# Performance work log

Measured on AMD Instinct MI355X. Metric: run time of the kernel, lower is better.

The kernel has to match this reference:

```python
import jax, jax.numpy as jnp
import numpy as np

B, S, C_IN, E, H, DFF = 16, 1024, 4, 128, 8, 512
C1 = E * 4
DH = E // H
EPS = 1e-5


def _layer_norm(x, g, b):
    m = x.mean(-1, keepdims=True)
    v = ((x - m) ** 2).mean(-1, keepdims=True)
    return (x - m) / jnp.sqrt(v + EPS) * g + b


def _forward(x, conv1_w, conv1_b, bn1_g, bn1_b, bn1_m, bn1_v,
             conv2_w, conv2_b, bn2_g, bn2_b, bn2_m, bn2_v,
             wq, wk, wv, rel_bias, ln_attn_g, ln_attn_b,
             ln1_g, ln1_b, ff_w1, ff_b1, ff_w2, ff_b2, ln2_g, ln2_b):
    b, s, _ = x.shape
    dn = ('NCHW', 'OIHW', 'NCHW')
    h = x.transpose(0, 2, 1)[:, None]                      # [B,1,4,S]
    # Conv2d(1, 512, [1,8], padding='same') -> torch pads (3,4) on width
    h = jax.lax.conv_general_dilated(h, conv1_w, (1, 1), [(0, 0), (3, 4)], dimension_numbers=dn)
    h = h + conv1_b[None, :, None, None]
    h = (h - bn1_m[None, :, None, None]) * (bn1_g / jnp.sqrt(bn1_v + EPS))[None, :, None, None] + bn1_b[None, :, None, None]
    h = jax.nn.gelu(h, approximate=False)                  # [B,512,4,S]
    # Conv2d(512, 128, [4,1], padding='valid') collapses channel axis
    h = jax.lax.conv_general_dilated(h, conv2_w, (1, 1), [(0, 0), (0, 0)], dimension_numbers=dn)
    h = h + conv2_b[None, :, None, None]
    h = (h - bn2_m[None, :, None, None]) * (bn2_g / jnp.sqrt(bn2_v + EPS))[None, :, None, None] + bn2_b[None, :, None, None]
    h = jax.nn.gelu(h, approximate=False)                  # [B,128,1,S]
    x_src = h[:, :, 0, :].transpose(0, 2, 1)               # [B,S,E]
    # tAPE fixed positional encoding (sin/cos scaled by E/S)
    pos = jnp.arange(s, dtype=x.dtype)[:, None]
    div = jnp.exp(jnp.arange(0, E, 2, dtype=x.dtype) * (-np.log(10000.0) / E))
    ang = pos * div * (E / s)
    pe = jnp.zeros((s, E), x.dtype).at[:, 0::2].set(jnp.sin(ang)).at[:, 1::2].set(jnp.cos(ang))
    xp = x_src + pe
    # eRPE attention (Attention_Rel_Scl): scale = emb_size**-0.5, bias added POST-softmax
    q = (xp @ wq.T).reshape(b, s, H, DH).transpose(0, 2, 1, 3)
    k = (xp @ wk.T).reshape(b, s, H, DH).transpose(0, 2, 1, 3)
    v = (xp @ wv.T).reshape(b, s, H, DH).transpose(0, 2, 1, 3)
    attn = jax.nn.softmax(jnp.einsum('bhid,bhjd->bhij', q, k) * (E ** -0.5), axis=-1)
    idx = jnp.arange(s)[:, None] - jnp.arange(s)[None, :] + (s - 1)   # [S,S] in [0, 2S-2]
    attn = attn + rel_bias[idx].transpose(2, 0, 1)[None]   # [1,H,S,S]
    o = jnp.einsum('bhij,bhjd->bhid', attn, v).transpose(0, 2, 1, 3).reshape(b, s, E)
    o = _layer_norm(o, ln_attn_g, ln_attn_b)               # to_out = LayerNorm
    att = _layer_norm(x_src + o, ln1_g, ln1_b)
    ff = jax.nn.relu(att @ ff_w1.T + ff_b1) @ ff_w2.T + ff_b2
    out = _layer_norm(att + ff, ln2_g, ln2_b)
    return out.mean(axis=1)                                # GAP + flatten -> [B,E]


def setup_inputs():
    key = jax.random.key(0)
    ks = jax.random.split(key, 16)
    f32 = jnp.float32
    return {
        'x': jax.random.normal(ks[0], (B, S, C_IN), f32),
        'conv1_w': jax.random.normal(ks[1], (C1, 1, 1, 8), f32) * 0.1,
        'conv1_b': jnp.zeros((C1,), f32),
        'bn1_g': jnp.ones((C1,), f32), 'bn1_b': jnp.zeros((C1,), f32),
        'bn1_m': jax.random.normal(ks[2], (C1,), f32) * 0.01,
        'bn1_v': jax.random.uniform(ks[3], (C1,), f32, 0.5, 1.5),
        'conv2_w': jax.random.normal(ks[4], (E, C1, C_IN, 1), f32) * 0.02,
        'conv2_b': jnp.zeros((E,), f32),
        'bn2_g': jnp.ones((E,), f32), 'bn2_b': jnp.zeros((E,), f32),
        'bn2_m': jax.random.normal(ks[5], (E,), f32) * 0.01,
        'bn2_v': jax.random.uniform(ks[6], (E,), f32, 0.5, 1.5),
        'wq': jax.random.normal(ks[7], (E, E), f32) * (E ** -0.5),
        'wk': jax.random.normal(ks[8], (E, E), f32) * (E ** -0.5),
        'wv': jax.random.normal(ks[9], (E, E), f32) * (E ** -0.5),
        'rel_bias': jax.random.normal(ks[10], (2 * S - 1, H), f32) * 0.02,
        'ln_attn_g': jnp.ones((E,), f32), 'ln_attn_b': jnp.zeros((E,), f32),
        'ln1_g': jnp.ones((E,), f32), 'ln1_b': jnp.zeros((E,), f32),
        'ff_w1': jax.random.normal(ks[11], (DFF, E), f32) * (E ** -0.5),
        'ff_b1': jnp.zeros((DFF,), f32),
        'ff_w2': jax.random.normal(ks[12], (E, DFF), f32) * (DFF ** -0.5),
        'ff_b2': jnp.zeros((E,), f32),
        'ln2_g': jnp.ones((E,), f32), 'ln2_b': jnp.zeros((E,), f32),
    }


def reference(x, conv1_w, conv1_b, bn1_g, bn1_b, bn1_m, bn1_v,
              conv2_w, conv2_b, bn2_g, bn2_b, bn2_m, bn2_v,
              wq, wk, wv, rel_bias, ln_attn_g, ln_attn_b,
              ln1_g, ln1_b, ff_w1, ff_b1, ff_w2, ff_b2, ln2_g, ln2_b):
    return _forward(x, conv1_w, conv1_b, bn1_g, bn1_b, bn1_m, bn1_v,
                    conv2_w, conv2_b, bn2_g, bn2_b, bn2_m, bn2_v,
                    wq, wk, wv, rel_bias, ln_attn_g, ln_attn_b,
                    ln1_g, ln1_b, ff_w1, ff_b1, ff_w2, ff_b2, ln2_g, ln2_b)
```

## Files before the change

kernel.cpp:

```cpp
#include <hip/hip_runtime.h>
#include <hip/hip_bf16.h>
#include <math.h>

using bf16 = __hip_bfloat16;
typedef unsigned short u16;
typedef unsigned int u32;
typedef const float* __restrict__ cfp;
typedef const u16* __restrict__ cbu;

typedef __attribute__((ext_vector_type(8))) short short8v;
typedef __attribute__((ext_vector_type(4))) float f32x4;
typedef __attribute__((ext_vector_type(16))) float f32x16;

static constexpr int kS = 1024, kE = 128, kH = 8, kDH = 16, kDFF = 512;
static constexpr float kEps = 1e-5f;

__device__ __forceinline__ float geluf(float x) { return 0.5f * x * (1.f + erff(x * 0.70710678118654752f)); }
__device__ __forceinline__ float gelu_fast(float x) {
  float x2 = x * x;
  float u2 = 1.5957691216057308f * x * fmaf(0.044715f, x2, 1.f);
  float t = __expf(u2);
  return fmaf(-x, __frcp_rn(t + 1.f), x);
}
__device__ __forceinline__ u16 f2b(float f) {
  u32 u = __float_as_uint(f);
  u32 r = (u + 0x7FFFu + ((u >> 16) & 1u)) >> 16;
  return (u16)r;
}

template<int N> __device__ __forceinline__ void wait_vmcnt() {
  asm volatile("s_waitcnt vmcnt(%0)" :: "n"(N) : "memory");
  __builtin_amdgcn_sched_barrier(0);
}

__global__ __launch_bounds__(256) void setup_kernel(
    cfp x, cfp w1, cfp c1b, cfp g1, cfp b1, cfp m1, cfp v1, u16* __restrict__ Abuf,
    cfp w2, u16* __restrict__ w2b, cfp relb, u16* __restrict__ T,
    cfp fw2, u16* __restrict__ w2fb, float* __restrict__ dout,
    cfp wq, cfp wk, cfp wv, u16* __restrict__ wqkvb,
    cfp fw1, u16* __restrict__ w1fb) {
  int tid = threadIdx.x;
  if (blockIdx.x < 2048) {
    __shared__ float xs[15][4];
    int row0 = blockIdx.x * 8;
    int b = row0 >> 10, s0 = row0 & 1023;
    if (tid < 15) {
      int gs = s0 - 3 + tid;
      float4 xv = (gs >= 0 && gs < kS) ? ((const float4*)x)[b * kS + gs]
                                       : make_float4(0.f, 0.f, 0.f, 0.f);
      xs[tid][0] = xv.x; xs[tid][1] = xv.y; xs[tid][2] = xv.z; xs[tid][3] = xv.w;
    }
    __syncthreads();

    float w[2][8], sc[2], ofs[2], cb[2];
#pragma unroll
    for (int cc = 0; cc < 2; ++cc) {
      int cx = tid * 2 + cc;
#pragma unroll
      for (int t = 0; t < 8; ++t) w[cc][t] = w1[cx * 8 + t];
      sc[cc] = g1[cx] * __frsqrt_rn(v1[cx] + kEps);
      ofs[cc] = b1[cx] - m1[cx] * sc[cc];
      cb[cc] = c1b[cx];
    }

    for (int rl = 0; rl < 8; ++rl) {
      float ev[8];
#pragma unroll
      for (int cc = 0; cc < 2; ++cc) {
#pragma unroll
        for (int rr = 0; rr < 4; ++rr) {
          float h = cb[cc];
#pragma unroll
          for (int t = 0; t < 8; ++t) h += xs[rl + t][rr] * w[cc][t];
          ev[cc * 4 + rr] = gelu_fast(h * sc[cc] + ofs[cc]);
        }
      }
      uint4 pk;
      asm("v_cvt_pk_bf16_f32 %0, %1, %2" : "=v"(pk.x) : "v"(ev[0]), "v"(ev[1]));
      asm("v_cvt_pk_bf16_f32 %0, %1, %2" : "=v"(pk.y) : "v"(ev[2]), "v"(ev[3]));
      asm("v_cvt_pk_bf16_f32 %0, %1, %2" : "=v"(pk.z) : "v"(ev[4]), "v"(ev[5]));
      asm("v_cvt_pk_bf16_f32 %0, %1, %2" : "=v"(pk.w) : "v"(ev[6]), "v"(ev[7]));
      int ck = (tid & ~7) | ((tid & 7) ^ (rl & 7));
      *(uint4*)(Abuf + (size_t)(row0 + rl) * 2048 + ck * 8) = pk;
    }
    return;
  }

  int bid = blockIdx.x - 2048;
  if (bid < 128) {
    int n = bid, ck = tid;
    const float* src = w2 + (size_t)n * 2048 + (size_t)ck * 8;
    float4 a = *(const float4*)src;
    float4 b = *(const float4*)(src + 4);
    short8v sv;
    sv[0] = (short)f2b(a.x); sv[1] = (short)f2b(a.y);
    sv[2] = (short)f2b(a.z); sv[3] = (short)f2b(a.w);
    sv[4] = (short)f2b(b.x); sv[5] = (short)f2b(b.y);
    sv[6] = (short)f2b(b.z); sv[7] = (short)f2b(b.w);
    int cd = (ck & ~7) | ((ck & 7) ^ (n & 7));
    *(short8v*)(w2b + (size_t)n * 2048 + cd * 8) = sv;
  } else if (bid < 380) {
    int idx = (bid - 128) * 4 + (tid >> 6);
    int l = tid & 63;
    int h = idx / 126, t = idx - h * 126;
    int lr = l & 15, lg = l >> 4;
    short8v v;
#pragma unroll
    for (int e = 0; e < 8; ++e) {
      int ix = 16 * t + 31 + lr - 8 * lg - e;
      v[e] = (short)f2b(relb[ix * 8 + h]);
    }
    *(short8v*)(T + ((size_t)(h * 126 + t) * 64 + l) * 8) = v;
  } else if (bid < 412) {
    int n = (bid - 380) * 4 + (tid >> 6);
    int ck = tid & 63;
    const float* src = fw2 + (size_t)n * 512 + (size_t)ck * 8;
    float4 a = *(const float4*)src;
    float4 b = *(const float4*)(src + 4);
    short8v sv;
    sv[0] = (short)f2b(a.x); sv[1] = (short)f2b(a.y);
    sv[2] = (short)f2b(a.z); sv[3] = (short)f2b(a.w);
    sv[4] = (short)f2b(b.x); sv[5] = (short)f2b(b.y);
    sv[6] = (short)f2b(b.z); sv[7] = (short)f2b(b.w);
    int cd = (ck & ~7) | ((ck & 7) ^ (n & 7));
    *(short8v*)(w2fb + (size_t)n * 512 + cd * 8) = sv;
  } else if (bid < 413) {
#pragma unroll
    for (int e = 0; e < 8; ++e) dout[tid * 8 + e] = 0.f;
  } else if (bid < 437) {
    int g = (bid - 413) * 256 + tid;
    int z = g >> 11, local = g & 2047;
    const float* src = ((z == 0) ? wq : (z == 1) ? wk : wv) + (size_t)local * 8;
    float4 a = *(const float4*)src;
    float4 b = *(const float4*)(src + 4);
    short8v sv;
    sv[0] = (short)f2b(a.x); sv[1] = (short)f2b(a.y);
    sv[2] = (short)f2b(a.z); sv[3] = (short)f2b(a.w);
    sv[4] = (short)f2b(b.x); sv[5] = (short)f2b(b.y);
    sv[6] = (short)f2b(b.z); sv[7] = (short)f2b(b.w);
    *(short8v*)(wqkvb + (size_t)z * 16384 + local * 8) = sv;
  } else {
    int g = (bid - 437) * 256 + tid;
    const float* src = fw1 + (size_t)g * 8;
    float4 a = *(const float4*)src;
    float4 b = *(const float4*)(src + 4);
    short8v sv;
    sv[0] = (short)f2b(a.x); sv[1] = (short)f2b(a.y);
    sv[2] = (short)f2b(a.z); sv[3] = (short)f2b(a.w);
    sv[4] = (short)f2b(b.x); sv[5] = (short)f2b(b.y);
    sv[6] = (short)f2b(b.z); sv[7] = (short)f2b(b.w);
    *(short8v*)(w1fb + (size_t)g * 8) = sv;
  }
}

__global__ __launch_bounds__(256, 2) void convgemm_kernel(
    const u16* __restrict__ Abuf, const u16* __restrict__ w2b,
    cfp c2b, cfp g2, cfp b2, cfp m2, cfp v2,
    float* __restrict__ xsrc, u16* __restrict__ xpeb) {
  __shared__ short8v lds[3840];
  const int tid = threadIdx.x;
  const int mtile = blockIdx.x;
  const int wid = tid >> 6, lane = tid & 63;
  const int lrow = lane & 15, lk = lane >> 4;
  const int m0w = (wid & 1) * 16, n0w = (wid >> 1) * 64;

  float scn[4], cc[4], dv[4];
#pragma unroll
  for (int ni = 0; ni < 4; ++ni) {
    int n = n0w + ni * 16 + lrow;
    scn[ni] = g2[n] * __frsqrt_rn(v2[n] + kEps);
    cc[ni] = (c2b[n] - m2[n]) * scn[ni] + b2[n];
    dv[ni] = __expf((float)(n >> 1) * (-0.14391156824963732f)) * 0.125f;
  }

  f32x4 acc[4];
#pragma unroll
  for (int ni = 0; ni < 4; ++ni) acc[ni] = (f32x4){0.f, 0.f, 0.f, 0.f};

  const int q = wid * 64 + lane;
  const u16* aG = Abuf + (size_t)(mtile * 32 + (q >> 3)) * 2048 + (q & 7) * 8;

  auto stage = [&](int t) {
    int buf = t % 3;
    short8v* A = lds + buf * 1280;
    __builtin_amdgcn_global_load_lds(
        (const __attribute__((address_space(1))) void*)(aG + t * 64),
        (__attribute__((address_space(3))) void*)(A + wid * 64), 16, 0, 0);
#pragma unroll
    for (int r = 0; r < 4; ++r) {
      int qq = r * 256 + q;
      const u16* g = w2b + (size_t)(qq >> 3) * 2048 + t * 64 + (qq & 7) * 8;
      __builtin_amdgcn_global_load_lds(
          (const __attribute__((address_space(1))) void*)g,
          (__attribute__((address_space(3))) void*)(A + 256 + r * 256 + wid * 64), 16, 0, 0);
    }
  };

  auto compute = [&](int t) {
    int buf = t % 3;
    const short8v* A = lds + buf * 1280;
    const short8v* B = A + 256;
#pragma unroll
    for (int ks = 0; ks < 2; ++ks) {
      int ar = m0w + lrow;
      u32 ao = ((u32)(ar * 128 + ks * 64 + lk * 16)) ^ ((u32)((ar & 7) << 4));
      short8v af = A[ao >> 4];
#pragma unroll
      for (int ni = 0; ni < 4; ++ni) {
        int br = n0w + ni * 16 + lrow;
        u32 bo = ((u32)(br * 128 + ks * 64 + lk * 16)) ^ ((u32)((br & 7) << 4));
        short8v bf = B[bo >> 4];
        acc[ni] = __builtin_amdgcn_mfma_f32_16x16x32_bf16(af, bf, acc[ni], 0, 0, 0);
      }
    }
  };

  stage(0); stage(1); stage(2);
  for (int t = 0; t < 30; ++t) {
    wait_vmcnt<10>();
    __builtin_amdgcn_s_barrier();
    __builtin_amdgcn_sched_barrier(0);
    compute(t);
    asm volatile("" ::: "memory");
    __builtin_amdgcn_s_barrier();
    __builtin_amdgcn_sched_barrier(0);
    if (t <= 28) stage(t + 3);
  }
  wait_vmcnt<5>();
  __builtin_amdgcn_s_barrier();
  __builtin_amdgcn_sched_barrier(0);
  compute(30);
  asm volatile("" ::: "memory");
  __builtin_amdgcn_s_barrier();
  __builtin_amdgcn_sched_barrier(0);
  wait_vmcnt<0>();
  __builtin_amdgcn_s_barrier();
  __builtin_amdgcn_sched_barrier(0);
  compute(31);

#pragma unroll
  for (int ni = 0; ni < 4; ++ni) {
    int n = n0w + ni * 16 + lrow;
#pragma unroll
    for (int r = 0; r < 4; ++r) {
      int grow = mtile * 32 + m0w + lk * 4 + r;
      float gv = geluf(acc[ni][r] * scn[ni] + cc[ni]);
      xsrc[(size_t)grow * kE + n] = gv;
      int s = grow & 1023;
      float ang = (float)s * dv[ni];
      float pe = (n & 1) ? __cosf(ang) : __sinf(ang);
      xpeb[(size_t)grow * kE + n] = f2b(gv + pe);
    }
  }
}

template<int ASRC, int MODE, int KTOT, int BM>
__global__ __launch_bounds__(256, 4) void gemm_kernel(
    const void* __restrict__ Ap, cbu Wf,
    cfp p0, cbu p1, cbu p2,
    void* __restrict__ Out, cfp res, int mbase) {
  constexpr int MI = BM / 32;
  __shared__ short8v Ab[BM * 8];
  __shared__ short8v Bb[512];

  int tid = threadIdx.x;
  int mtile = blockIdx.x, ntile = blockIdx.y;

  cbu Wsel = Wf;
  if (MODE == 1) Wsel = (blockIdx.z == 0) ? Wf : ((blockIdx.z == 1) ? p1 : p2);

  int wid = tid >> 6, lane = tid & 63;
  int m0w = (wid >> 1) * (BM / 2), n0w = (wid & 1) * 32;
  int lrow = lane & 15, lk = lane >> 4;

  f32x4 acc[MI][2];
#pragma unroll
  for (int mi = 0; mi < MI; ++mi)
#pragma unroll
    for (int ni = 0; ni < 2; ++ni) acc[mi][ni] = (f32x4){0.f, 0.f, 0.f, 0.f};

  for (int k0 = 0; k0 < KTOT; k0 += 64) {
    __syncthreads();
#pragma unroll
    for (int c = 0; c < BM / 32; ++c) {
      int chunk = tid + 256 * c;
      int row = chunk >> 3, kc = chunk & 7;
      int arow = mtile * BM + row;
      u32 off = ((u32)(row * 128 + kc * 16)) ^ ((u32)((row & 7) << 4));
      const u16* As = (const u16*)Ap + (size_t)arow * KTOT + k0 + kc * 8;
      Ab[off >> 4] = *(const short8v*)As;
    }
#pragma unroll
    for (int c = 0; c < 2; ++c) {
      int chunk = tid + 256 * c;
      int row = chunk >> 3, kc = chunk & 7;
      const u16* Wp = Wsel + (size_t)(ntile * 64 + row) * KTOT + k0 + kc * 8;
      u32 off = ((u32)(row * 128 + kc * 16)) ^ ((u32)((row & 7) << 4));
      Bb[off >> 4] = *(const short8v*)Wp;
    }
    __syncthreads();
#pragma unroll
    for (int ks = 0; ks < 2; ++ks) {
      short8v af[MI], bfr[2];
#pragma unroll
      for (int mi = 0; mi < MI; ++mi) {
        int row = m0w + mi * 16 + lrow;
        u32 off = ((u32)(row * 128 + ks * 64 + lk * 16)) ^ ((u32)((row & 7) << 4));
        af[mi] = Ab[off >> 4];
      }
#pragma unroll
      for (int ni = 0; ni < 2; ++ni) {
        int row = n0w + ni * 16 + lrow;
        u32 off = ((u32)(row * 128 + ks * 64 + lk * 16)) ^ ((u32)((row & 7) << 4));
        bfr[ni] = Bb[off >> 4];
      }
#pragma unroll
      for (int mi = 0; mi < MI; ++mi)
#pragma unroll
        for (int ni = 0; ni < 2; ++ni)
          acc[mi][ni] = __builtin_amdgcn_mfma_f32_16x16x32_bf16(af[mi], bfr[ni], acc[mi][ni], 0, 0, 0);
    }
  }

  const float qsc = 0.088388347648318447f * 1.4426950408889634f;
#pragma unroll
  for (int ni = 0; ni < 2; ++ni) {
    int n = ntile * 64 + n0w + ni * 16 + lrow;
    float c0 = 0.f;
    if (MODE == 2) c0 = p0[n];
#pragma unroll
    for (int mi = 0; mi < MI; ++mi) {
#pragma unroll
      for (int r = 0; r < 4; ++r) {
        int grow = mbase + mtile * BM + m0w + mi * 16 + lk * 4 + r;
        float val = acc[mi][ni][r];
        if (MODE == 1) {
          if (blockIdx.z == 0) val *= qsc;
          int s = grow & 1023, b_ = grow >> 10;
          u16* ob = (u16*)Out + (size_t)blockIdx.z * 2097152;
          ob[(((size_t)(b_ * kH + (n >> 4))) * kS + s) * kDH + (n & 15)] = f2b(val);
        } else if (MODE == 2) {
          int np = (n & ~56) | ((((n >> 3) ^ grow) & 7) << 3);
          ((u16*)Out)[(size_t)grow * kDFF + np] = f2b(fmaxf(val + c0, 0.f));
        }
      }
    }
  }
}

__global__ __launch_bounds__(256, 2) void ff2ln_kernel(
    const u16* __restrict__ Abuf, const u16* __restrict__ w2fb,
    cfp fb2, cfp l2g, cfp l2b, cfp res, float* __restrict__ dout) {
  __shared__ short8v lds[3840];
  __shared__ float st1[2][32], st2[2][32];
  __shared__ float red[128];
  const int tid = threadIdx.x;
  const int mtile = blockIdx.x;
  const int wid = tid >> 6, lane = tid & 63;
  const int lrow = lane & 15, lk = lane >> 4;
  const int m0w = (wid & 1) * 16, n0w = (wid >> 1) * 64;
  if (tid < 128) red[tid] = 0.f;

  float c0[4], gg[4], bb[4];
#pragma unroll
  for (int ni = 0; ni < 4; ++ni) {
    int n = n0w + ni * 16 + lrow;
    c0[ni] = fb2[n]; gg[ni] = l2g[n]; bb[ni] = l2b[n];
  }

  f32x4 acc[4];
#pragma unroll
  for (int ni = 0; ni < 4; ++ni) acc[ni] = (f32x4){0.f, 0.f, 0.f, 0.f};

  const int q = wid * 64 + lane;
  const u16* aG = Abuf + (size_t)(mtile * 32 + (q >> 3)) * 512 + (q & 7) * 8;

  auto stage = [&](int t) {
    int buf = t % 3;
    short8v* A = lds + buf * 1280;
    __builtin_amdgcn_global_load_lds(
        (const __attribute__((address_space(1))) void*)(aG + t * 64),
        (__attribute__((address_space(3))) void*)(A + wid * 64), 16, 0, 0);
#pragma unroll
    for (int r = 0; r < 4; ++r) {
      int qq = r * 256 + q;
      const u16* g = w2fb + (size_t)(qq >> 3) * 512 + t * 64 + (qq & 7) * 8;
      __builtin_amdgcn_global_load_lds(
          (const __attribute__((address_space(1))) void*)g,
          (__attribute__((address_space(3))) void*)(A + 256 + r * 256 + wid * 64), 16, 0, 0);
    }
  };

  auto compute = [&](int t) {
    int buf = t % 3;
    const short8v* A = lds + buf * 1280;
    const short8v* B = A + 256;
#pragma unroll
    for (int ks = 0; ks < 2; ++ks) {
      int ar = m0w + lrow;
      u32 ao = ((u32)(ar * 128 + ks * 64 + lk * 16)) ^ ((u32)((ar & 7) << 4));
      short8v af = A[ao >> 4];
#pragma unroll
      for (int ni = 0; ni < 4; ++ni) {
        int br = n0w + ni * 16 + lrow;
        u32 bo = ((u32)(br * 128 + ks * 64 + lk * 16)) ^ ((u32)((br & 7) << 4));
        short8v bf = B[bo >> 4];
        acc[ni] = __builtin_amdgcn_mfma_f32_16x16x32_bf16(af, bf, acc[ni], 0, 0, 0);
      }
    }
  };

  stage(0); stage(1); stage(2);
  for (int t = 0; t < 6; ++t) {
    wait_vmcnt<10>();
    __builtin_amdgcn_s_barrier();
    __builtin_amdgcn_sched_barrier(0);
    compute(t);
    asm volatile("" ::: "memory");
    __builtin_amdgcn_s_barrier();
    __builtin_amdgcn_sched_barrier(0);
    if (t <= 4) stage(t + 3);
  }
  wait_vmcnt<5>();
  __builtin_amdgcn_s_barrier();
  __builtin_amdgcn_sched_barrier(0);
  compute(6);
  asm volatile("" ::: "memory");
  __builtin_amdgcn_s_barrier();
  __builtin_amdgcn_sched_barrier(0);
  wait_vmcnt<0>();
  __builtin_amdgcn_s_barrier();
  __builtin_amdgcn_sched_barrier(0);
  compute(7);

  float y[4][4];
  float s1[4] = {0.f, 0.f, 0.f, 0.f}, s2[4] = {0.f, 0.f, 0.f, 0.f};
#pragma unroll
  for (int ni = 0; ni < 4; ++ni) {
    int n = n0w + ni * 16 + lrow;
#pragma unroll
    for (int r = 0; r < 4; ++r) {
      int grow = mtile * 32 + m0w + lk * 4 + r;
      float v = acc[ni][r] + c0[ni] + res[(size_t)grow * kE + n];
      y[ni][r] = v;
      s1[r] += v;
      s2[r] += v * v;
    }
  }
#pragma unroll
  for (int r = 0; r < 4; ++r) {
    for (int off = 1; off < 16; off <<= 1) {
      s1[r] += __shfl_xor(s1[r], off);
      s2[r] += __shfl_xor(s2[r], off);
    }
  }
  __syncthreads();
  if (lrow == 0) {
#pragma unroll
    for (int r = 0; r < 4; ++r) {
      int ridx = m0w + lk * 4 + r;
      st1[wid >> 1][ridx] = s1[r];
      st2[wid >> 1][ridx] = s2[r];
    }
  }
  __syncthreads();
  float colsum[4] = {0.f, 0.f, 0.f, 0.f};
#pragma unroll
  for (int r = 0; r < 4; ++r) {
    int ridx = m0w + lk * 4 + r;
    float t1 = st1[0][ridx] + st1[1][ridx];
    float t2 = st2[0][ridx] + st2[1][ridx];
    float mean = t1 * (1.f / 128.f);
    float var = t2 * (1.f / 128.f) - mean * mean;
    float inv = __frsqrt_rn(var + kEps);
#pragma unroll
    for (int ni = 0; ni < 4; ++ni)
      colsum[ni] += (y[ni][r] - mean) * inv * gg[ni] + bb[ni];
  }
#pragma unroll
  for (int ni = 0; ni < 4; ++ni) {
    colsum[ni] += __shfl_xor(colsum[ni], 16);
    colsum[ni] += __shfl_xor(colsum[ni], 32);
  }
  if (lk == 0) {
#pragma unroll
    for (int ni = 0; ni < 4; ++ni)
      atomicAdd(&red[n0w + ni * 16 + lrow], colsum[ni]);
  }
  __syncthreads();
  int b = mtile >> 5;
  if (tid < 128) atomicAdd(&dout[b * kE + tid], red[tid] * (1.f / 1024.f));
}

__global__ __launch_bounds__(512, 2) void attn_kernel(
    const u16* __restrict__ qb, const u16* __restrict__ kb,
    const u16* __restrict__ vb, const u16* __restrict__ rbT,
    float* __restrict__ o) {
  __shared__ u16 Vsh[16 * 1032];
  __shared__ u16 Pt[8][1280];

  int tid = threadIdx.x;
  int bid = blockIdx.x;
  int quarter = bid >> 7;
  int bb = (bid >> 3) & 15;
  int h = bid & 7;
  size_t base = (size_t)(bb * kH + h) * (kS * kDH);

  for (int j = tid; j < 1024; j += 512) {
    const uint4* src = (const uint4*)(vb + base + j * 16);
    uint4 a = src[0], b = src[1];
    u32 wv[8] = {a.x, a.y, a.z, a.w, b.x, b.y, b.z, b.w};
#pragma unroll
    for (int p = 0; p < 8; ++p) {
      Vsh[(2 * p) * 1032 + j]     = (u16)(wv[p] & 0xFFFFu);
      Vsh[(2 * p + 1) * 1032 + j] = (u16)(wv[p] >> 16);
    }
  }
  __syncthreads();

  int w = tid >> 6, l = tid & 63;
  int lr = l & 15, lg = l >> 4;
  int q32 = l & 31, hi = l >> 5;
  u16* P = Pt[w];
  int q0w = quarter * 256 + w * 32;
  int tbase = (q0w + 992) >> 4;
  const u16* rbh = rbT + (size_t)h * 126 * 512;

  short8v qf = *(const short8v*)(qb + base + (size_t)(q0w + q32) * 16 + hi * 8);
  short8v ones;
#pragma unroll
  for (int e = 0; e < 8; ++e) ones[e] = (short)0x3F80;

  f32x4 acc_e[2], acc_rb[2], acc_l[2];
#pragma unroll
  for (int qt = 0; qt < 2; ++qt) {
    acc_e[qt] = (f32x4){0.f, 0.f, 0.f, 0.f};
    acc_rb[qt] = (f32x4){0.f, 0.f, 0.f, 0.f};
    acc_l[qt] = (f32x4){0.f, 0.f, 0.f, 0.f};
  }
  const f32x16 z16 = {0.f,0.f,0.f,0.f,0.f,0.f,0.f,0.f,0.f,0.f,0.f,0.f,0.f,0.f,0.f,0.f};

  const u16* kfp = kb + base + (size_t)q32 * 16 + hi * 8;
  const u16* rfp = rbh + (size_t)tbase * 512 + l * 8;

  short8v kf_c = *(const short8v*)kfp;
  short8v rf0_c = *(const short8v*)rfp;
  short8v rf1_c = *(const short8v*)(rfp + 512);

  const int wswz = (q32 >> 3) & 3;
  const int c0r = lg ^ ((lr >> 3) & 3);
  const int c1r = lg ^ (((16 + lr) >> 3) & 3);

  for (int jb = 0; jb < 32; ++jb) {
    short8v kf_n, rf0_n, rf1_n;
    if (jb < 31) {
      kf_n = *(const short8v*)(kfp + (size_t)(jb + 1) * 512);
      const u16* rp = rfp - (size_t)(jb + 1) * 1024;
      rf0_n = *(const short8v*)rp;
      rf1_n = *(const short8v*)(rp + 512);
    }
    f32x16 s = __builtin_amdgcn_mfma_f32_32x32x16_bf16(kf_c, qf, z16, 0, 0, 0);
    float ev[16];
#pragma unroll
    for (int r = 0; r < 16; ++r) ev[r] = __builtin_amdgcn_exp2f(s[r]);
#pragma unroll
    for (int rq = 0; rq < 4; ++rq) {
      u32 p0, p1;
      asm("v_cvt_pk_bf16_f32 %0, %1, %2" : "=v"(p0) : "v"(ev[4 * rq]), "v"(ev[4 * rq + 1]));
      asm("v_cvt_pk_bf16_f32 %0, %1, %2" : "=v"(p1) : "v"(ev[4 * rq + 2]), "v"(ev[4 * rq + 3]));
      *(uint2*)(P + q32 * 40 + (rq ^ wswz) * 8 + hi * 4) = make_uint2(p0, p1);
    }
    short8v vf = *(const short8v*)(Vsh + lr * 1032 + jb * 32 + lg * 8);
    {
      short8v pf0 = *(const short8v*)(P + lr * 40 + c0r * 8);
      acc_e[0]  = __builtin_amdgcn_mfma_f32_16x16x32_bf16(pf0, vf, acc_e[0], 0, 0, 0);
      acc_l[0]  = __builtin_amdgcn_mfma_f32_16x16x32_bf16(pf0, ones, acc_l[0], 0, 0, 0);
      acc_rb[0] = __builtin_amdgcn_mfma_f32_16x16x32_bf16(rf0_c, vf, acc_rb[0], 0, 0, 0);
      short8v pf1 = *(const short8v*)(P + (16 + lr) * 40 + c1r * 8);
      acc_e[1]  = __builtin_amdgcn_mfma_f32_16x16x32_bf16(pf1, vf, acc_e[1], 0, 0, 0);
      acc_l[1]  = __builtin_amdgcn_mfma_f32_16x16x32_bf16(pf1, ones, acc_l[1], 0, 0, 0);
      acc_rb[1] = __builtin_amdgcn_mfma_f32_16x16x32_bf16(rf1_c, vf, acc_rb[1], 0, 0, 0);
    }
    if (jb < 31) {
      kf_c = kf_n; rf0_c = rf0_n; rf1_c = rf1_n;
    }
  }

#pragma unroll
  for (int qt = 0; qt < 2; ++qt) {
#pragma unroll
    for (int r = 0; r < 4; ++r) {
      int qloc = qt * 16 + lg * 4 + r;
      int row = q0w + qloc;
      o[(size_t)(bb * kS + row) * kE + h * kDH + lr] =
          acc_e[qt][r] / acc_l[qt][r] + acc_rb[qt][r];
    }
  }
}

__global__ __launch_bounds__(256) void ln_kernel(
    cfp o, cfp xsrc, cfp lag, cfp lab, cfp l1g, cfp l1b,
    float* __restrict__ att, u16* __restrict__ attb) {
  int row = blockIdx.x * 4 + (threadIdx.x >> 6);
  int lane = threadIdx.x & 63;
  float2 a = ((const float2*)(o + (size_t)row * kE))[lane];
  float sum = a.x + a.y;
  for (int off = 1; off < 64; off <<= 1) sum += __shfl_xor(sum, off);
  float mean = sum * (1.f / 128.f);
  float d0 = a.x - mean, d1 = a.y - mean;
  float ss = d0 * d0 + d1 * d1;
  for (int off = 1; off < 64; off <<= 1) ss += __shfl_xor(ss, off);
  float inv = 1.f / sqrtf(ss * (1.f / 128.f) + kEps);
  float t0 = d0 * inv * lag[2 * lane] + lab[2 * lane];
  float t1 = d1 * inv * lag[2 * lane + 1] + lab[2 * lane + 1];
  float2 xv = ((const float2*)(xsrc + (size_t)row * kE))[lane];
  t0 += xv.x; t1 += xv.y;
  float sum2 = t0 + t1;
  for (int off = 1; off < 64; off <<= 1) sum2 += __shfl_xor(sum2, off);
  float mean2 = sum2 * (1.f / 128.f);
  float e0 = t0 - mean2, e1 = t1 - mean2;
  float ss2 = e0 * e0 + e1 * e1;
  for (int off = 1; off < 64; off <<= 1) ss2 += __shfl_xor(ss2, off);
  float inv2 = 1.f / sqrtf(ss2 * (1.f / 128.f) + kEps);
  float r0 = e0 * inv2 * l1g[2 * lane] + l1b[2 * lane];
  float r1 = e1 * inv2 * l1g[2 * lane + 1] + l1b[2 * lane + 1];
  ((float2*)(att + (size_t)row * kE))[lane] = make_float2(r0, r1);
  ((u32*)attb)[(size_t)row * 64 + lane] = (u32)f2b(r0) | ((u32)f2b(r1) << 16);
}

extern "C" void kernel_launch(void* const* d_in, const int* in_sizes, int n_in,
                              void* d_out, int out_size, void* d_ws, size_t ws_size,
                              hipStream_t stream) {
  const float* wf[27];
  for (int i = 0; i < n_in && i < 27; ++i) wf[i] = (const float*)d_in[i];

  float* ws = (float*)d_ws;
  float* xsrc  = ws;
  float* att   = xsrc + 2097152;
  float* qkv0  = att + 2097152;
  float* ext   = qkv0 + 3145728;
  float* o     = ext + 1048576;
  u16* xpeb    = (u16*)(o + 2097152);
  u16* w2b     = xpeb + 2097152;
  u16* rbT     = w2b + 262144;
  u16* w2fb    = rbT + 516096;
  u16* Abuf    = w2fb + 65536;
  u16* wqkvb   = Abuf + 33554432;
  u16* w1fb    = wqkvb + 49152;

  u16* qb = (u16*)qkv0;
  u16* kb = qb + 2097152;
  u16* vb = kb + 2097152;
  u16* ff1b = (u16*)qkv0;
  u16* attb = xpeb;
  float* doutf = (float*)d_out;

  setup_kernel<<<2517, 256, 0, stream>>>(
      wf[0], wf[1], wf[2], wf[3], wf[4], wf[5], wf[6], Abuf,
      wf[7], w2b, wf[16], rbT, wf[23], w2fb, doutf,
      wf[13], wf[14], wf[15], wqkvb, wf[21], w1fb);

  convgemm_kernel<<<512, 256, 0, stream>>>(
      Abuf, w2b, wf[8], wf[9], wf[10], wf[11], wf[12], xsrc, xpeb);

  gemm_kernel<3, 1, 128, 64><<<dim3(256, 2, 3), 256, 0, stream>>>(
      xpeb, wqkvb, nullptr, wqkvb + 16384, wqkvb + 32768, qb, nullptr, 0);

  attn_kernel<<<512, 512, 0, stream>>>(qb, kb, vb, rbT, o);
  ln_kernel<<<4096, 256, 0, stream>>>(o, xsrc, wf[17], wf[18], wf[19], wf[20], att, attb);

  gemm_kernel<3, 2, 128, 64><<<dim3(256, 8), 256, 0, stream>>>(
      attb, w1fb, wf[22], nullptr, nullptr, ff1b, nullptr, 0);

  ff2ln_kernel<<<512, 256, 0, stream>>>(ff1b, w2fb, wf[24], wf[25], wf[26], att, doutf);
}
```

Before: 109.5 us.

## Fuse conv1+BN+GELU into the conv2 GEMM, building A tiles in LDS

Removes the 64MB bf16 intermediate Abuf that the setup kernel wrote and the conv GEMM read back. Each conv GEMM block now computes its conv1+BN+GELU A-tile on the fly from x and w1 held in LDS, double-buffered alongside the triple-buffered async B loads. The weight prep moves to a smaller prep kernel. This trades a large HBM round trip for extra ALU work per tile and higher LDS use, which may lower occupancy.

After: 113.9 us. +4.1%, slower.

```diff
diff --git a/kernel.cpp b/kernel.cpp
--- a/kernel.cpp
+++ b/kernel.cpp
@@ -32,61 +32,18 @@
   asm volatile("s_waitcnt vmcnt(%0)" :: "n"(N) : "memory");
   __builtin_amdgcn_sched_barrier(0);
 }
-
-__global__ __launch_bounds__(256) void setup_kernel(
-    cfp x, cfp w1, cfp c1b, cfp g1, cfp b1, cfp m1, cfp v1, u16* __restrict__ Abuf,
+__device__ __forceinline__ void wait_lgkm0() {
+  asm volatile("s_waitcnt lgkmcnt(0)" ::: "memory");
+  __builtin_amdgcn_sched_barrier(0);
+}
+
+__global__ __launch_bounds__(256) void prep_kernel(
     cfp w2, u16* __restrict__ w2b, cfp relb, u16* __restrict__ T,
     cfp fw2, u16* __restrict__ w2fb, float* __restrict__ dout,
     cfp wq, cfp wk, cfp wv, u16* __restrict__ wqkvb,
     cfp fw1, u16* __restrict__ w1fb) {
+  int bid = blockIdx.x;
   int tid = threadIdx.x;
-  if (blockIdx.x < 2048) {
-    __shared__ float xs[15][4];
-    int row0 = blockIdx.x * 8;
-    int b = row0 >> 10, s0 = row0 & 1023;
-    if (tid < 15) {
-      int gs = s0 - 3 + tid;
-      float4 xv = (gs >= 0 && gs < kS) ? ((const float4*)x)[b * kS + gs]
-                                       : make_float4(0.f, 0.f, 0.f, 0.f);
-      xs[tid][0] = xv.x; xs[tid][1] = xv.y; xs[tid][2] = xv.z; xs[tid][3] = xv.w;
-    }
-    __syncthreads();
-
-    float w[2][8], sc[2], ofs[2], cb[2];
-#pragma unroll
-    for (int cc = 0; cc < 2; ++cc) {
-      int cx = tid * 2 + cc;
-#pragma unroll
-      for (int t = 0; t < 8; ++t) w[cc][t] = w1[cx * 8 + t];
-      sc[cc] = g1[cx] * __frsqrt_rn(v1[cx] + kEps);
-      ofs[cc] = b1[cx] - m1[cx] * sc[cc];
-      cb[cc] = c1b[cx];
-    }
-
-    for (int rl = 0; rl < 8; ++rl) {
-      float ev[8];
-#pragma unroll
-      for (int cc = 0; cc < 2; ++cc) {
-#pragma unroll
-        for (int rr = 0; rr < 4; ++rr) {
-          float h = cb[cc];
-#pragma unroll
-          for (int t = 0; t < 8; ++t) h += xs[rl + t][rr] * w[cc][t];
-          ev[cc * 4 + rr] = gelu_fast(h * sc[cc] + ofs[cc]);
-        }
-      }
-      uint4 pk;
-      asm("v_cvt_pk_bf16_f32 %0, %1, %2" : "=v"(pk.x) : "v"(ev[0]), "v"(ev[1]));
-      asm("v_cvt_pk_bf16_f32 %0, %1, %2" : "=v"(pk.y) : "v"(ev[2]), "v"(ev[3]));
-      asm("v_cvt_pk_bf16_f32 %0, %1, %2" : "=v"(pk.z) : "v"(ev[4]), "v"(ev[5]));
-      asm("v_cvt_pk_bf16_f32 %0, %1, %2" : "=v"(pk.w) : "v"(ev[6]), "v"(ev[7]));
-      int ck = (tid & ~7) | ((tid & 7) ^ (rl & 7));
-      *(uint4*)(Abuf + (size_t)(row0 + rl) * 2048 + ck * 8) = pk;
-    }
-    return;
-  }
-
-  int bid = blockIdx.x - 2048;
   if (bid < 128) {
     int n = bid, ck = tid;
     const float* src = w2 + (size_t)n * 2048 + (size_t)ck * 8;
@@ -153,16 +110,42 @@
   }
 }
 
-__global__ __launch_bounds__(256, 2) void convgemm_kernel(
-    const u16* __restrict__ Abuf, const u16* __restrict__ w2b,
+__global__ __launch_bounds__(256, 2) void convfused_kernel(
+    cfp x, cfp w1, cfp c1b, cfp g1, cfp b1, cfp m1, cfp v1,
+    const u16* __restrict__ w2b,
     cfp c2b, cfp g2, cfp b2, cfp m2, cfp v2,
     float* __restrict__ xsrc, u16* __restrict__ xpeb) {
-  __shared__ short8v lds[3840];
+  __shared__ short8v Bb[3072];
+  __shared__ short8v Aa[512];
+  __shared__ float w1s[512][9];
+  __shared__ float2 cns[512];
+  __shared__ float xsh[40][4];
+
   const int tid = threadIdx.x;
   const int mtile = blockIdx.x;
   const int wid = tid >> 6, lane = tid & 63;
   const int lrow = lane & 15, lk = lane >> 4;
   const int m0w = (wid & 1) * 16, n0w = (wid >> 1) * 64;
+  const int arow = tid >> 3, akc = tid & 7;
+
+  for (int i = tid; i < 512; i += 256) {
+    const float4* s4 = (const float4*)(w1 + i * 8);
+    float4 a = s4[0], b4 = s4[1];
+    w1s[i][0] = a.x;  w1s[i][1] = a.y;  w1s[i][2] = a.z;  w1s[i][3] = a.w;
+    w1s[i][4] = b4.x; w1s[i][5] = b4.y; w1s[i][6] = b4.z; w1s[i][7] = b4.w;
+    float sc = g1[i] * __frsqrt_rn(v1[i] + kEps);
+    cns[i] = make_float2(sc, fmaf(c1b[i], sc, b1[i] - m1[i] * sc));
+  }
+  {
+    int row0 = mtile * 32;
+    int b = row0 >> 10, s0 = row0 & 1023;
+    if (tid < 39) {
+      int gs = s0 - 3 + tid;
+      float4 xv = (gs >= 0 && gs < kS) ? ((const float4*)x)[b * kS + gs]
+                                       : make_float4(0.f, 0.f, 0.f, 0.f);
+      xsh[tid][0] = xv.x; xsh[tid][1] = xv.y; xsh[tid][2] = xv.z; xsh[tid][3] = xv.w;
+    }
+  }
 
   float scn[4], cc[4], dv[4];
 #pragma unroll
@@ -177,29 +160,56 @@
 #pragma unroll
   for (int ni = 0; ni < 4; ++ni) acc[ni] = (f32x4){0.f, 0.f, 0.f, 0.f};
 
+  __syncthreads();
+
+  float xr[8][4];
+#pragma unroll
+  for (int tp = 0; tp < 8; ++tp)
+#pragma unroll
+    for (int r = 0; r < 4; ++r) xr[tp][r] = xsh[arow + tp][r];
+
+  auto buildA = [&](int t) {
+    short8v* A = Aa + (t & 1) * 256;
+    int c1a = t * 16 + akc * 2;
+    float2 cn0 = cns[c1a], cn1 = cns[c1a + 1];
+    float ev[8];
+#pragma unroll
+    for (int c2 = 0; c2 < 2; ++c2) {
+      int cx = c1a + c2;
+      float sc_ = c2 ? cn1.x : cn0.x;
+      float of_ = c2 ? cn1.y : cn0.y;
+#pragma unroll
+      for (int r = 0; r < 4; ++r) {
+        float hs = 0.f;
+#pragma unroll
+        for (int tp = 0; tp < 8; ++tp) hs = fmaf(xr[tp][r], w1s[cx][tp], hs);
+        ev[c2 * 4 + r] = gelu_fast(fmaf(hs, sc_, of_));
+      }
+    }
+    uint4 pk;
+    asm("v_cvt_pk_bf16_f32 %0, %1, %2" : "=v"(pk.x) : "v"(ev[0]), "v"(ev[1]));
+    asm("v_cvt_pk_bf16_f32 %0, %1, %2" : "=v"(pk.y) : "v"(ev[2]), "v"(ev[3]));
+    asm("v_cvt_pk_bf16_f32 %0, %1, %2" : "=v"(pk.z) : "v"(ev[4]), "v"(ev[5]));
+    asm("v_cvt_pk_bf16_f32 %0, %1, %2" : "=v"(pk.w) : "v"(ev[6]), "v"(ev[7]));
+    *(uint4*)(A + arow * 8 + (akc ^ (arow & 7))) = pk;
+  };
+
   const int q = wid * 64 + lane;
-  const u16* aG = Abuf + (size_t)(mtile * 32 + (q >> 3)) * 2048 + (q & 7) * 8;
-
-  auto stage = [&](int t) {
-    int buf = t % 3;
-    short8v* A = lds + buf * 1280;
-    __builtin_amdgcn_global_load_lds(
-        (const __attribute__((address_space(1))) void*)(aG + t * 64),
-        (__attribute__((address_space(3))) void*)(A + wid * 64), 16, 0, 0);
+  auto stageB = [&](int t) {
+    short8v* B = Bb + (t % 3) * 1024;
 #pragma unroll
     for (int r = 0; r < 4; ++r) {
       int qq = r * 256 + q;
       const u16* g = w2b + (size_t)(qq >> 3) * 2048 + t * 64 + (qq & 7) * 8;
       __builtin_amdgcn_global_load_lds(
           (const __attribute__((address_space(1))) void*)g,
-          (__attribute__((address_space(3))) void*)(A + 256 + r * 256 + wid * 64), 16, 0, 0);
+          (__attribute__((address_space(3))) void*)(B + r * 256 + wid * 64), 16, 0, 0);
     }
   };
 
   auto compute = [&](int t) {
-    int buf = t % 3;
-    const short8v* A = lds + buf * 1280;
-    const short8v* B = A + 256;
+    const short8v* A = Aa + (t & 1) * 256;
+    const short8v* B = Bb + (t % 3) * 1024;
 #pragma unroll
     for (int ks = 0; ks < 2; ++ks) {
       int ar = m0w + lrow;
@@ -215,18 +225,27 @@
     }
   };
 
-  stage(0); stage(1); stage(2);
+  buildA(0);
+  stageB(0); stageB(1); stageB(2);
+  wait_lgkm0();
+  __builtin_amdgcn_s_barrier();
+  __builtin_amdgcn_sched_barrier(0);
+
   for (int t = 0; t < 30; ++t) {
-    wait_vmcnt<10>();
+    buildA(t + 1);
+    wait_vmcnt<8>();
+    wait_lgkm0();
     __builtin_amdgcn_s_barrier();
     __builtin_amdgcn_sched_barrier(0);
     compute(t);
     asm volatile("" ::: "memory");
     __builtin_amdgcn_s_barrier();
     __builtin_amdgcn_sched_barrier(0);
-    if (t <= 28) stage(t + 3);
-  }
-  wait_vmcnt<5>();
+    if (t <= 28) stageB(t + 3);
+  }
+  buildA(31);
+  wait_vmcnt<4>();
+  wait_lgkm0();
   __builtin_amdgcn_s_barrier();
   __builtin_amdgcn_sched_barrier(0);
   compute(30);
@@ -644,8 +663,7 @@
   u16* w2b     = xpeb + 2097152;
   u16* rbT     = w2b + 262144;
   u16* w2fb    = rbT + 516096;
-  u16* Abuf    = w2fb + 65536;
-  u16* wqkvb   = Abuf + 33554432;
+  u16* wqkvb   = w2fb + 65536;
   u16* w1fb    = wqkvb + 49152;
 
   u16* qb = (u16*)qkv0;
@@ -655,13 +673,12 @@
   u16* attb = xpeb;
   float* doutf = (float*)d_out;
 
-  setup_kernel<<<2517, 256, 0, stream>>>(
-      wf[0], wf[1], wf[2], wf[3], wf[4], wf[5], wf[6], Abuf,
-      wf[7], w2b, wf[16], rbT, wf[23], w2fb, doutf,
-      wf[13], wf[14], wf[15], wqkvb, wf[21], w1fb);
-
-  convgemm_kernel<<<512, 256, 0, stream>>>(
-      Abuf, w2b, wf[8], wf[9], wf[10], wf[11], wf[12], xsrc, xpeb);
+  prep_kernel<<<469, 256, 0, stream>>>(wf[7], w2b, wf[16], rbT, wf[23], w2fb, doutf,
+                                       wf[13], wf[14], wf[15], wqkvb, wf[21], w1fb);
+
+  convfused_kernel<<<512, 256, 0, stream>>>(
+      wf[0], wf[1], wf[2], wf[3], wf[4], wf[5], wf[6],
+      w2b, wf[8], wf[9], wf[10], wf[11], wf[12], xsrc, xpeb);
 
   gemm_kernel<3, 1, 128, 64><<<dim3(256, 2, 3), 256, 0, stream>>>(
       xpeb, wqkvb, nullptr, wqkvb + 16384, wqkvb + 32768, qb, nullptr, 0);
```
